# Kernel tuning notes

Measured on AMD Instinct MI355X. Metric: run time of the kernel, lower is better.

## Reference

```python
import jax, jax.numpy as jnp
import numpy as np

GRID_SIZE = 10
DEGREE = 3


def bspline_basis(x, grid_size=GRID_SIZE, degree=DEGREE):
    """Cox-de Boor B-spline basis on a uniform grid over [-1, 1].
    x: (...,) -> (..., grid_size + degree)
    """
    h = 2.0 / grid_size
    # extended knot vector, length grid_size + 2*degree + 1
    knots = jnp.arange(-degree, grid_size + degree + 1, dtype=x.dtype) * h - 1.0
    # keep inputs inside the grid support (standard KAN practice)
    x = jnp.clip(x, -1.0, 1.0 - 1e-6)
    xe = x[..., None]
    b = ((xe >= knots[:-1]) & (xe < knots[1:])).astype(x.dtype)  # degree-0, (..., K-1)
    for d in range(1, degree + 1):
        left = (xe - knots[: -(d + 1)]) / (knots[d:-1] - knots[: -(d + 1)]) * b[..., :-1]
        right = (knots[d + 1:] - xe) / (knots[d + 1:] - knots[1:-d]) * b[..., 1:]
        b = left + right
    return b  # (..., grid_size + degree)


def setup_inputs() -> dict:
    key = jax.random.key(0)
    k1, k2, k3 = jax.random.split(key, 3)
    B, S, IN, OUT, E = 4, 2048, 256, 256, 8
    n_basis = GRID_SIZE + DEGREE
    x = jax.random.normal(k1, (B, S, IN), dtype=jnp.float32)
    coeff = jax.random.normal(k2, (E, n_basis), dtype=jnp.float32) * 0.1
    gating_weights = jax.random.normal(k3, (IN, OUT, E), dtype=jnp.float32)
    return {"x": x, "coeff": coeff, "gating_weights": gating_weights}


def reference(x, coeff, gating_weights):
    # spline experts: elementwise basis eval, then per-expert linear combo
    basis = bspline_basis(x)                              # (B, S, I, n_basis)
    expert_outputs = jnp.einsum('bsin,en->bsie', basis, coeff)  # (B, S, I, E)
    gates = jax.nn.softmax(gating_weights, axis=-1)       # (I, O, E)
    out = jnp.einsum('bsie,ioe->bso', expert_outputs, gates)
    return out
```

## Files before the change

### kernel.cpp

```cpp
#include <hip/hip_runtime.h>

typedef __attribute__((ext_vector_type(8))) short short8;
typedef __attribute__((ext_vector_type(4))) float f32x4;

#define IN_DIM 256
#define OUT_DIM 256
#define NB 16
#define KDIM (IN_DIM * NB)
#define TM 64
#define TN 64
#define BK 128
#define STEPS 32
#define ABUF 16384

__device__ __forceinline__ unsigned short f2bf(float f) {
  union { float f; unsigned int u; } v; v.f = f;
  unsigned int r = v.u + 0x7fffu + ((v.u >> 16) & 1u);
  return (unsigned short)(r >> 16);
}

__device__ __forceinline__ void spline_row(float xv, unsigned* d) {
  float xc = fminf(fmaxf(xv, -1.0f), 1.0f - 1e-6f);
  float u = (xc + 1.0f) * 5.0f;
  int c = (int)u;
  c = c > 9 ? 9 : (c < 0 ? 0 : c);
  float tt = u - (float)c;
  float omt = 1.0f - tt;
  float t2 = tt * tt, t3 = t2 * tt;
  float b0 = omt * omt * omt * (1.0f / 6.0f);
  float b1 = (3.0f * t3 - 6.0f * t2 + 4.0f) * (1.0f / 6.0f);
  float b2 = (-3.0f * t3 + 3.0f * t2 + 3.0f * tt + 1.0f) * (1.0f / 6.0f);
  float b3 = t3 * (1.0f / 6.0f);
  unsigned h0 = f2bf(b0), h1 = f2bf(b1), h2 = f2bf(b2), h3 = f2bf(b3);
  const int a = c >> 1;
  const bool odd = (c & 1) != 0;
  unsigned p01 = h0 | (h1 << 16);
  unsigned p23 = h2 | (h3 << 16);
  unsigned A0 = odd ? (h0 << 16) : p01;
  unsigned A1 = odd ? (h1 | (h2 << 16)) : p23;
  unsigned A2 = odd ? h3 : 0u;
#pragma unroll
  for (int j = 0; j < 8; ++j) {
    unsigned v = (j == a) ? A0 : 0u;
    v = (j == a + 1) ? A1 : v;
    v = (j == a + 2) ? A2 : v;
    d[j] = v;
  }
}

__global__ __launch_bounds__(256) void kan_prep(const float* __restrict__ coeff,
                                                const float* __restrict__ gw,
                                                unsigned short* __restrict__ BmT) {
  __shared__ float csh[104];
  __shared__ unsigned short tile[16][256];
  const int t = threadIdx.x;
  if (t < 104) csh[t] = coeff[t];
  __syncthreads();
  const int otile = blockIdx.x, itile = blockIdx.y;
  const int il = t >> 4, ol = t & 15;
  const int i = itile * 16 + il;
  const int o = otile * 16 + ol;
  const float* g = gw + (size_t)(i * OUT_DIM + o) * 8;
  float4 g0 = *(const float4*)g;
  float4 g1 = *(const float4*)(g + 4);
  float ge[8] = {g0.x, g0.y, g0.z, g0.w, g1.x, g1.y, g1.z, g1.w};
  float mx = ge[0];
#pragma unroll
  for (int e = 1; e < 8; ++e) mx = fmaxf(mx, ge[e]);
  float p[8]; float s = 0.f;
#pragma unroll
  for (int e = 0; e < 8; ++e) { p[e] = __expf(ge[e] - mx); s += p[e]; }
  const float inv = 1.0f / s;
  unsigned short row[16];
#pragma unroll
  for (int n = 0; n < 13; ++n) {
    float w = 0.f;
#pragma unroll
    for (int e = 0; e < 8; ++e) w += p[e] * csh[e * 13 + n];
    row[n] = f2bf(w * inv);
  }
  row[13] = 0; row[14] = 0; row[15] = 0;
  int4* dst = (int4*)&tile[ol][il * 16];
  dst[0] = *(const int4*)&row[0];
  dst[1] = *(const int4*)&row[8];
  __syncthreads();
  const int oo = t >> 4, ck = t & 15;
  int4 v0 = *(const int4*)&tile[oo][ck * 16];
  int4 v1 = *(const int4*)&tile[oo][ck * 16 + 8];
  int4* out4 = (int4*)(BmT + (size_t)(otile * 16 + oo) * KDIM + itile * 256 + ck * 16);
  out4[0] = v0;
  out4[1] = v1;
}

__global__ __launch_bounds__(256, 2) void kan_gemm(const float* __restrict__ x,
                                                   const unsigned short* __restrict__ BmT,
                                                   float* __restrict__ out) {
  __shared__ unsigned short Ash[2][TM * BK];

  const int t = threadIdx.x;
  const int lane = t & 63;
  const int wave = t >> 6;
  const int wm = wave >> 1, wn = wave & 1;
  const int mb = blockIdx.x * TM;
  const int ob = blockIdx.y * TN;

  const int r = t >> 2, ip = t & 3;
  const float* xp = x + (size_t)(mb + r) * IN_DIM + 2 * ip;
  char* const ab0 = (char*)&Ash[0][0] + r * 256;
  const int msw = r & 7;
  const int aw0 = ((4 * ip + 0) ^ msw) << 4;
  const int aw1 = ((4 * ip + 1) ^ msw) << 4;
  const int aw2 = ((4 * ip + 2) ^ msw) << 4;
  const int aw3 = ((4 * ip + 3) ^ msw) << 4;

  const int rl = lane & 15, qd = lane >> 4;

  const unsigned short* bp[2];
#pragma unroll
  for (int f = 0; f < 2; ++f)
    bp[f] = BmT + (size_t)(ob + wn * 32 + f * 16 + rl) * KDIM + qd * 8;

  int aadr[4][2];
#pragma unroll
  for (int ks = 0; ks < 4; ++ks)
#pragma unroll
    for (int f = 0; f < 2; ++f) {
      const int ro = wm * 32 + f * 16 + rl;
      aadr[ks][f] = ro * 256 + (((qd | (ks << 2)) ^ (ro & 7)) << 4);
    }

  f32x4 acc[2][2];
#pragma unroll
  for (int a = 0; a < 2; ++a)
#pragma unroll
    for (int b = 0; b < 2; ++b) acc[a][b] = (f32x4){0.f, 0.f, 0.f, 0.f};

  {
    float2 xv = *(const float2*)xp;
    unsigned d[8];
    spline_row(xv.x, d);
    *(int4*)(ab0 + aw0) = *(const int4*)&d[0];
    *(int4*)(ab0 + aw1) = *(const int4*)&d[4];
    spline_row(xv.y, d);
    *(int4*)(ab0 + aw2) = *(const int4*)&d[0];
    *(int4*)(ab0 + aw3) = *(const int4*)&d[4];
    asm volatile("s_waitcnt lgkmcnt(0)" ::: "memory");
    __builtin_amdgcn_sched_barrier(0);
    __builtin_amdgcn_s_barrier();
  }

  for (int s = 0; s < STEPS; ++s) {
    const int cur = s & 1;
    float2 xn = {0.f, 0.f};
    if (s + 1 < STEPS) xn = *(const float2*)(xp + 8 * (s + 1));
    const char* Ac = (const char*)&Ash[0][0] + cur * ABUF;
#pragma unroll
    for (int ks = 0; ks < 4; ++ks) {
      short8 bfr[2], af[2];
#pragma unroll
      for (int f = 0; f < 2; ++f) bfr[f] = *(const short8*)(bp[f] + s * 128 + ks * 32);
#pragma unroll
      for (int f = 0; f < 2; ++f) af[f] = *(const short8*)(Ac + aadr[ks][f]);
#pragma unroll
      for (int mf = 0; mf < 2; ++mf)
#pragma unroll
        for (int nf = 0; nf < 2; ++nf)
          acc[mf][nf] = __builtin_amdgcn_mfma_f32_16x16x32_bf16(af[mf], bfr[nf], acc[mf][nf], 0, 0, 0);
    }
    if (s + 1 < STEPS) {
      unsigned d[8];
      char* an = ab0 + (1 - cur) * ABUF;
      spline_row(xn.x, d);
      *(int4*)(an + aw0) = *(const int4*)&d[0];
      *(int4*)(an + aw1) = *(const int4*)&d[4];
      spline_row(xn.y, d);
      *(int4*)(an + aw2) = *(const int4*)&d[0];
      *(int4*)(an + aw3) = *(const int4*)&d[4];
    }
    asm volatile("s_waitcnt lgkmcnt(0)" ::: "memory");
    __builtin_amdgcn_sched_barrier(0);
    __builtin_amdgcn_s_barrier();
  }

#pragma unroll
  for (int mf = 0; mf < 2; ++mf)
#pragma unroll
    for (int nf = 0; nf < 2; ++nf)
#pragma unroll
      for (int q = 0; q < 4; ++q) {
        int row = mb + wm * 32 + mf * 16 + (qd << 2) + q;
        int col = ob + wn * 32 + nf * 16 + rl;
        out[(size_t)row * OUT_DIM + col] = acc[mf][nf][q];
      }
}

extern "C" void kernel_launch(void* const* d_in, const int* in_sizes, int n_in,
                              void* d_out, int out_size, void* d_ws, size_t ws_size,
                              hipStream_t stream) {
  const float* x     = (const float*)d_in[0];
  const float* coeff = (const float*)d_in[1];
  const float* gw    = (const float*)d_in[2];
  float* out = (float*)d_out;
  unsigned short* BmT = (unsigned short*)d_ws;

  kan_prep<<<dim3(16, 16), dim3(256), 0, stream>>>(coeff, gw, BmT);
  dim3 grid(8192 / TM, OUT_DIM / TN);
  kan_gemm<<<grid, dim3(256), 0, stream>>>(x, BmT, out);
}
```

Baseline: 131.0 us.

## Build spline A fragments in registers and drop LDS staging and barriers

Each lane now evaluates the B-spline basis directly into its MFMA A-operand fragment from x values read straight from global memory. This removes the shared-memory double buffer, its swizzled stores and loads, and the per-step block barriers. B fragments and x are prefetched one step ahead in registers using ping-pong buffers. In exchange, spline evaluation is repeated across the two N-waves, each wave reads x redundantly, and register pressure rises.

```diff
diff --git a/kernel.cpp b/kernel.cpp
--- a/kernel.cpp
+++ b/kernel.cpp
@@ -9,43 +9,12 @@
 #define KDIM (IN_DIM * NB)
 #define TM 64
 #define TN 64
-#define BK 128
 #define STEPS 32
-#define ABUF 16384
 
 __device__ __forceinline__ unsigned short f2bf(float f) {
   union { float f; unsigned int u; } v; v.f = f;
   unsigned int r = v.u + 0x7fffu + ((v.u >> 16) & 1u);
   return (unsigned short)(r >> 16);
-}
-
-__device__ __forceinline__ void spline_row(float xv, unsigned* d) {
-  float xc = fminf(fmaxf(xv, -1.0f), 1.0f - 1e-6f);
-  float u = (xc + 1.0f) * 5.0f;
-  int c = (int)u;
-  c = c > 9 ? 9 : (c < 0 ? 0 : c);
-  float tt = u - (float)c;
-  float omt = 1.0f - tt;
-  float t2 = tt * tt, t3 = t2 * tt;
-  float b0 = omt * omt * omt * (1.0f / 6.0f);
-  float b1 = (3.0f * t3 - 6.0f * t2 + 4.0f) * (1.0f / 6.0f);
-  float b2 = (-3.0f * t3 + 3.0f * t2 + 3.0f * tt + 1.0f) * (1.0f / 6.0f);
-  float b3 = t3 * (1.0f / 6.0f);
-  unsigned h0 = f2bf(b0), h1 = f2bf(b1), h2 = f2bf(b2), h3 = f2bf(b3);
-  const int a = c >> 1;
-  const bool odd = (c & 1) != 0;
-  unsigned p01 = h0 | (h1 << 16);
-  unsigned p23 = h2 | (h3 << 16);
-  unsigned A0 = odd ? (h0 << 16) : p01;
-  unsigned A1 = odd ? (h1 | (h2 << 16)) : p23;
-  unsigned A2 = odd ? h3 : 0u;
-#pragma unroll
-  for (int j = 0; j < 8; ++j) {
-    unsigned v = (j == a) ? A0 : 0u;
-    v = (j == a + 1) ? A1 : v;
-    v = (j == a + 2) ? A2 : v;
-    d[j] = v;
-  }
 }
 
 __global__ __launch_bounds__(256) void kan_prep(const float* __restrict__ coeff,
@@ -92,94 +61,125 @@
   out4[1] = v1;
 }
 
+__device__ __forceinline__ short8 spline_granule(float xv, int g) {
+  float xc = fminf(fmaxf(xv, -1.0f), 1.0f - 1e-6f);
+  float u = (xc + 1.0f) * 5.0f;
+  int c = (int)u;
+  c = c > 9 ? 9 : (c < 0 ? 0 : c);
+  float tt = u - (float)c;
+  float omt = 1.0f - tt;
+  float t2 = tt * tt, t3 = t2 * tt;
+  float b0 = omt * omt * omt * (1.0f / 6.0f);
+  float b1 = (3.0f * t3 - 6.0f * t2 + 4.0f) * (1.0f / 6.0f);
+  float b2 = (-3.0f * t3 + 3.0f * t2 + 3.0f * tt + 1.0f) * (1.0f / 6.0f);
+  float b3 = t3 * (1.0f / 6.0f);
+  unsigned h0 = f2bf(b0), h1 = f2bf(b1), h2 = f2bf(b2), h3 = f2bf(b3);
+  const int a = c >> 1;
+  const bool odd = (c & 1) != 0;
+  unsigned A0 = odd ? (h0 << 16) : (h0 | (h1 << 16));
+  unsigned A1 = odd ? (h1 | (h2 << 16)) : (h2 | (h3 << 16));
+  unsigned A2 = odd ? h3 : 0u;
+  union { unsigned u[4]; short8 s; } r;
+  const int base = g * 4;
+#pragma unroll
+  for (int j = 0; j < 4; ++j) {
+    const int jj = base + j;
+    unsigned v = (jj == a) ? A0 : 0u;
+    v = (jj == a + 1) ? A1 : v;
+    v = (jj == a + 2) ? A2 : v;
+    r.u[j] = v;
+  }
+  return r.s;
+}
+
+struct XS { float4 r0l, r0h, r1l, r1h; };
+struct BS { short8 v[4][2]; };
+
+__device__ __forceinline__ void load_x(const float* xr0, const float* xr1, int s, XS& o) {
+  const int sc = (s < STEPS) ? s : STEPS - 1;
+  o.r0l = *(const float4*)(xr0 + sc * 8);
+  o.r0h = *(const float4*)(xr0 + sc * 8 + 4);
+  o.r1l = *(const float4*)(xr1 + sc * 8);
+  o.r1h = *(const float4*)(xr1 + sc * 8 + 4);
+}
+__device__ __forceinline__ void load_b(const unsigned short* bp0, const unsigned short* bp1,
+                                       int s, BS& o) {
+  const int sc = (s < STEPS) ? s : STEPS - 1;
+#pragma unroll
+  for (int ks = 0; ks < 4; ++ks) {
+    o.v[ks][0] = *(const short8*)(bp0 + sc * 128 + ks * 32);
+    o.v[ks][1] = *(const short8*)(bp1 + sc * 128 + ks * 32);
+  }
+}
+
 __global__ __launch_bounds__(256, 2) void kan_gemm(const float* __restrict__ x,
                                                    const unsigned short* __restrict__ BmT,
                                                    float* __restrict__ out) {
-  __shared__ unsigned short Ash[2][TM * BK];
-
   const int t = threadIdx.x;
   const int lane = t & 63;
   const int wave = t >> 6;
   const int wm = wave >> 1, wn = wave & 1;
   const int mb = blockIdx.x * TM;
   const int ob = blockIdx.y * TN;
-
-  const int r = t >> 2, ip = t & 3;
-  const float* xp = x + (size_t)(mb + r) * IN_DIM + 2 * ip;
-  char* const ab0 = (char*)&Ash[0][0] + r * 256;
-  const int msw = r & 7;
-  const int aw0 = ((4 * ip + 0) ^ msw) << 4;
-  const int aw1 = ((4 * ip + 1) ^ msw) << 4;
-  const int aw2 = ((4 * ip + 2) ^ msw) << 4;
-  const int aw3 = ((4 * ip + 3) ^ msw) << 4;
-
   const int rl = lane & 15, qd = lane >> 4;
-
-  const unsigned short* bp[2];
-#pragma unroll
-  for (int f = 0; f < 2; ++f)
-    bp[f] = BmT + (size_t)(ob + wn * 32 + f * 16 + rl) * KDIM + qd * 8;
-
-  int aadr[4][2];
-#pragma unroll
-  for (int ks = 0; ks < 4; ++ks)
-#pragma unroll
-    for (int f = 0; f < 2; ++f) {
-      const int ro = wm * 32 + f * 16 + rl;
-      aadr[ks][f] = ro * 256 + (((qd | (ks << 2)) ^ (ro & 7)) << 4);
+  const int qdh = qd >> 1, qg = qd & 1;
+
+  const float* xr0 = x + (size_t)(mb + wm * 32 + rl) * IN_DIM;
+  const float* xr1 = xr0 + 16 * IN_DIM;
+  const unsigned short* bp0 = BmT + (size_t)(ob + wn * 32 + rl) * KDIM + qd * 8;
+  const unsigned short* bp1 = bp0 + (size_t)16 * KDIM;
+
+  f32x4 acc[2][2];
+#pragma unroll
+  for (int a = 0; a < 2; ++a)
+#pragma unroll
+    for (int b = 0; b < 2; ++b) acc[a][b] = (f32x4){0.f, 0.f, 0.f, 0.f};
+
+  XS xA, xB;
+  BS bA, bB;
+  load_x(xr0, xr1, 0, xA);
+  load_b(bp0, bp1, 0, bA);
+
+#pragma unroll 1
+  for (int s = 0; s < STEPS; s += 2) {
+    load_b(bp0, bp1, s + 1, bB);
+    load_x(xr0, xr1, s + 1, xB);
+#pragma unroll
+    for (int ks = 0; ks < 4; ++ks) {
+      const float c0 = (ks == 0) ? (qdh ? xA.r0l.y : xA.r0l.x)
+                     : (ks == 1) ? (qdh ? xA.r0l.w : xA.r0l.z)
+                     : (ks == 2) ? (qdh ? xA.r0h.y : xA.r0h.x)
+                                 : (qdh ? xA.r0h.w : xA.r0h.z);
+      const float c1 = (ks == 0) ? (qdh ? xA.r1l.y : xA.r1l.x)
+                     : (ks == 1) ? (qdh ? xA.r1l.w : xA.r1l.z)
+                     : (ks == 2) ? (qdh ? xA.r1h.y : xA.r1h.x)
+                                 : (qdh ? xA.r1h.w : xA.r1h.z);
+      const short8 a0 = spline_granule(c0, qg);
+      const short8 a1 = spline_granule(c1, qg);
+      acc[0][0] = __builtin_amdgcn_mfma_f32_16x16x32_bf16(a0, bA.v[ks][0], acc[0][0], 0, 0, 0);
+      acc[0][1] = __builtin_amdgcn_mfma_f32_16x16x32_bf16(a0, bA.v[ks][1], acc[0][1], 0, 0, 0);
+      acc[1][0] = __builtin_amdgcn_mfma_f32_16x16x32_bf16(a1, bA.v[ks][0], acc[1][0], 0, 0, 0);
+      acc[1][1] = __builtin_amdgcn_mfma_f32_16x16x32_bf16(a1, bA.v[ks][1], acc[1][1], 0, 0, 0);
     }
-
-  f32x4 acc[2][2];
-#pragma unroll
-  for (int a = 0; a < 2; ++a)
-#pragma unroll
-    for (int b = 0; b < 2; ++b) acc[a][b] = (f32x4){0.f, 0.f, 0.f, 0.f};
-
-  {
-    float2 xv = *(const float2*)xp;
-    unsigned d[8];
-    spline_row(xv.x, d);
-    *(int4*)(ab0 + aw0) = *(const int4*)&d[0];
-    *(int4*)(ab0 + aw1) = *(const int4*)&d[4];
-    spline_row(xv.y, d);
-    *(int4*)(ab0 + aw2) = *(const int4*)&d[0];
-    *(int4*)(ab0 + aw3) = *(const int4*)&d[4];
-    asm volatile("s_waitcnt lgkmcnt(0)" ::: "memory");
-    __builtin_amdgcn_sched_barrier(0);
-    __builtin_amdgcn_s_barrier();
-  }
-
-  for (int s = 0; s < STEPS; ++s) {
-    const int cur = s & 1;
-    float2 xn = {0.f, 0.f};
-    if (s + 1 < STEPS) xn = *(const float2*)(xp + 8 * (s + 1));
-    const char* Ac = (const char*)&Ash[0][0] + cur * ABUF;
+    load_b(bp0, bp1, s + 2, bA);
+    load_x(xr0, xr1, s + 2, xA);
 #pragma unroll
     for (int ks = 0; ks < 4; ++ks) {
-      short8 bfr[2], af[2];
-#pragma unroll
-      for (int f = 0; f < 2; ++f) bfr[f] = *(const short8*)(bp[f] + s * 128 + ks * 32);
-#pragma unroll
-      for (int f = 0; f < 2; ++f) af[f] = *(const short8*)(Ac + aadr[ks][f]);
-#pragma unroll
-      for (int mf = 0; mf < 2; ++mf)
-#pragma unroll
-        for (int nf = 0; nf < 2; ++nf)
-          acc[mf][nf] = __builtin_amdgcn_mfma_f32_16x16x32_bf16(af[mf], bfr[nf], acc[mf][nf], 0, 0, 0);
+      const float c0 = (ks == 0) ? (qdh ? xB.r0l.y : xB.r0l.x)
+                     : (ks == 1) ? (qdh ? xB.r0l.w : xB.r0l.z)
+                     : (ks == 2) ? (qdh ? xB.r0h.y : xB.r0h.x)
+                                 : (qdh ? xB.r0h.w : xB.r0h.z);
+      const float c1 = (ks == 0) ? (qdh ? xB.r1l.y : xB.r1l.x)
+                     : (ks == 1) ? (qdh ? xB.r1l.w : xB.r1l.z)
+                     : (ks == 2) ? (qdh ? xB.r1h.y : xB.r1h.x)
+                                 : (qdh ? xB.r1h.w : xB.r1h.z);
+      const short8 a0 = spline_granule(c0, qg);
+      const short8 a1 = spline_granule(c1, qg);
+      acc[0][0] = __builtin_amdgcn_mfma_f32_16x16x32_bf16(a0, bB.v[ks][0], acc[0][0], 0, 0, 0);
+      acc[0][1] = __builtin_amdgcn_mfma_f32_16x16x32_bf16(a0, bB.v[ks][1], acc[0][1], 0, 0, 0);
+      acc[1][0] = __builtin_amdgcn_mfma_f32_16x16x32_bf16(a1, bB.v[ks][0], acc[1][0], 0, 0, 0);
+      acc[1][1] = __builtin_amdgcn_mfma_f32_16x16x32_bf16(a1, bB.v[ks][1], acc[1][1], 0, 0, 0);
     }
-    if (s + 1 < STEPS) {
-      unsigned d[8];
-      char* an = ab0 + (1 - cur) * ABUF;
-      spline_row(xn.x, d);
-      *(int4*)(an + aw0) = *(const int4*)&d[0];
-      *(int4*)(an + aw1) = *(const int4*)&d[4];
-      spline_row(xn.y, d);
-      *(int4*)(an + aw2) = *(const int4*)&d[0];
-      *(int4*)(an + aw3) = *(const int4*)&d[4];
-    }
-    asm volatile("s_waitcnt lgkmcnt(0)" ::: "memory");
-    __builtin_amdgcn_sched_barrier(0);
-    __builtin_amdgcn_s_barrier();
   }
 
 #pragma unroll
@@ -188,7 +188,7 @@
     for (int nf = 0; nf < 2; ++nf)
 #pragma unroll
       for (int q = 0; q < 4; ++q) {
-        int row = mb + wm * 32 + mf * 16 + (qd << 2) + q;
+        int row = mb + wm * 32 + mf * 16 + qd * 4 + q;
         int col = ob + wn * 32 + nf * 16 + rl;
         out[(size_t)row * OUT_DIM + col] = acc[mf][nf][q];
       }
```

Result: slower. 175.5 us (+34.0%).
